# Performance work log

Hardware: AMD Instinct MI355X
Metric: run time of the kernel (lower is better)

The kernel has to match this reference:

```python
import jax, jax.numpy as jnp
import numpy as np
from jax import lax

G, CPG, KS, N = 8, 8, 3, 9  # groups, channels per group, kernel size, ks*ks


def conv2d(x, w, b=None, pad=1):
    y = lax.conv_general_dilated(x, w, (1, 1), [(pad, pad), (pad, pad)],
                                 dimension_numbers=('NCHW', 'OIHW', 'NCHW'))
    if b is not None:
        y = y + b[None, :, None, None]
    return y


def deform_group(x, f, pw, pb, mw, mb, cw):
    # x: sampled feature (anchor slice), f: offset source (motion slice); both (b,c,h,w)
    b, c, h, w = x.shape
    offset = conv2d(f, pw, pb)                      # (b, 2N, h, w)
    m = jax.nn.sigmoid(conv2d(f, mw, mb))           # (b, N, h, w) modulation
    off = jnp.transpose(offset, (0, 2, 3, 1))       # (b, h, w, 2N): first N rows(x), last N cols(y)
    rng = jnp.arange(-1, 2, dtype=x.dtype)
    pn_x = jnp.repeat(rng, KS)                      # kernel row offset, n = kr*3 + kc
    pn_y = jnp.tile(rng, KS)                        # kernel col offset
    p0_x = jnp.arange(1, h + 1, dtype=x.dtype)[:, None, None]  # base grid starts at 1 (padding=0 here)
    p0_y = jnp.arange(1, w + 1, dtype=x.dtype)[None, :, None]
    px = p0_x + pn_x + off[..., :N]                 # (b, h, w, N)
    py = p0_y + pn_y + off[..., N:]
    fx = jnp.floor(lax.stop_gradient(px))           # p.detach().floor() in the original
    fy = jnp.floor(lax.stop_gradient(py))
    qx_lt = jnp.clip(fx, 0, h - 1)
    qx_rb = jnp.clip(fx + 1, 0, h - 1)
    qy_lt = jnp.clip(fy, 0, w - 1)
    qy_rb = jnp.clip(fy + 1, 0, w - 1)
    px = jnp.clip(px, 0, h - 1)
    py = jnp.clip(py, 0, w - 1)
    g_lt = (1 + (qx_lt - px)) * (1 + (qy_lt - py))
    g_rb = (1 - (qx_rb - px)) * (1 - (qy_rb - py))
    g_lb = (1 + (qx_lt - px)) * (1 - (qy_rb - py))
    g_rt = (1 - (qx_rb - px)) * (1 + (qy_lt - py))
    x_flat = x.reshape(b, c, h * w)

    def gather(ix, iy):
        idx = (ix * w + iy).astype(jnp.int32).reshape(b, 1, -1)  # (b,1,h*w*N)
        return jnp.take_along_axis(x_flat, idx, axis=2).reshape(b, c, h, w, N)

    x_off = (g_lt[:, None] * gather(qx_lt, qy_lt) + g_rb[:, None] * gather(qx_rb, qy_rb)
             + g_lb[:, None] * gather(qx_lt, qy_rb) + g_rt[:, None] * gather(qx_rb, qy_lt))
    x_off = x_off * jnp.transpose(m, (0, 2, 3, 1))[:, None]      # apply modulation mask
    # fused equivalent of reshape to (b,c,h*3,w*3) + conv(k=3, stride=3, no bias)
    return jnp.einsum('bchwn,ocn->bohw', x_off, cw.reshape(cw.shape[0], c, N))


def reference(o, anchor, pw, pb, mw, mb, cw, w1, b1, w2, b2):
    b, C, h, w = anchor.shape
    xg = anchor.reshape(b, G, CPG, h, w).transpose(1, 0, 2, 3, 4)  # (G,b,c,h,w)
    fg = o.reshape(b, G, CPG, h, w).transpose(1, 0, 2, 3, 4)
    tg = jax.vmap(deform_group)(xg, fg, pw, pb, mw, mb, cw)        # (G,b,c,h,w)
    target = tg.transpose(1, 0, 2, 3, 4).reshape(b, C, h, w)
    target_ = jnp.concatenate([target, anchor], axis=1)            # (b,128,h,w)
    return target + conv2d(conv2d(target_, w1, b1), w2, b2)


def setup_inputs() -> dict:
    key = jax.random.key(0)
    ks = jax.random.split(key, 11)
    B, C, H, W = 4, 64, 128, 128
    return {
        'o': jax.random.normal(ks[0], (B, C, H, W), jnp.float32),
        'anchor': jax.random.normal(ks[1], (B, C, H, W), jnp.float32),
        'pw': jax.random.normal(ks[2], (G, 2 * N, CPG, 3, 3), jnp.float32) * 0.05,
        'pb': jax.random.normal(ks[3], (G, 2 * N), jnp.float32) * 0.05,
        'mw': jax.random.normal(ks[4], (G, N, CPG, 3, 3), jnp.float32) * 0.05,
        'mb': jax.random.normal(ks[5], (G, N), jnp.float32) * 0.05,
        'cw': jax.random.normal(ks[6], (G, CPG, CPG, 3, 3), jnp.float32) * 0.05,
        'w1': jax.random.normal(ks[7], (64, 128, 3, 3), jnp.float32) * 0.05,
        'b1': jax.random.normal(ks[8], (64,), jnp.float32) * 0.05,
        'w2': jax.random.normal(ks[9], (64, 64, 3, 3), jnp.float32) * 0.05,
        'b2': jax.random.normal(ks[10], (64,), jnp.float32) * 0.05,
    }
```

## Files before the change

### kernel.cpp

```cpp
#include <hip/hip_runtime.h>


typedef __attribute__((ext_vector_type(8))) short short8;
typedef __attribute__((ext_vector_type(4))) float float4v;
typedef __attribute__((ext_vector_type(2))) float float2v;

#define MFMA_B16(a, b, c) __builtin_amdgcn_mfma_f32_16x16x32_bf16(a, b, c, 0, 0, 0)

__device__ __forceinline__ ushort f2bf(float f) {
    union { float f; unsigned u; } v; v.f = f;
    unsigned r = v.u + 0x7FFFu + ((v.u >> 16) & 1u);
    return (ushort)(r >> 16);
}
__device__ __forceinline__ float bf2f(ushort h) {
    union { unsigned u; float f; } v; v.u = ((unsigned)h) << 16;
    return v.f;
}

__device__ __forceinline__ void tap_wo(int gy, int gx, int n,
                                       float ox, float oy, float mzv,
                                       float* W, int* O)
{
    int ky = n / 3, kx = n - ky * 3;
    float pxf = (float)(gy + ky) + ox;
    float pyf = (float)(gx + kx) + oy;
    float fx = floorf(pxf), fy = floorf(pyf);
    float qxl = fminf(fmaxf(fx, 0.f), 127.f);
    float qxr = fminf(fmaxf(fx + 1.f, 0.f), 127.f);
    float qyl = fminf(fmaxf(fy, 0.f), 127.f);
    float qyr = fminf(fmaxf(fy + 1.f, 0.f), 127.f);
    float pxc = fminf(fmaxf(pxf, 0.f), 127.f);
    float pyc = fminf(fmaxf(pyf, 0.f), 127.f);
    float glx = 1.f + (qxl - pxc), grx = 1.f - (qxr - pxc);
    float gly = 1.f + (qyl - pyc), gry = 1.f - (qyr - pyc);
    float mm = 1.f / (1.f + __expf(-mzv));
    W[0] = glx * gly * mm; W[1] = grx * gry * mm;
    W[2] = glx * gry * mm; W[3] = grx * gly * mm;
    int ixl = (int)qxl, ixr = (int)qxr, iyl = (int)qyl, iyr = (int)qyr;
    O[0] = ixl * 128 + iyl; O[1] = ixr * 128 + iyr;
    O[2] = ixl * 128 + iyr; O[3] = ixr * 128 + iyl;
}

__device__ __forceinline__ short8 interp4(const float* W, const short8* cv)
{
    union U { short8 s; uint4 u; };
    uint4 c[4];
    #pragma unroll
    for (int j = 0; j < 4; ++j) { U t; t.s = cv[j]; c[j] = t.u; }
    U out;
    #pragma unroll
    for (int p = 0; p < 4; ++p) {
        float2v acc = {0.f, 0.f};
        #pragma unroll
        for (int j = 0; j < 4; ++j) {
            unsigned d = (&c[j].x)[p];
            float2v cc = {__uint_as_float(d << 16),
                          __uint_as_float(d & 0xffff0000u)};
            float2v Wv = {W[j], W[j]};
            acc = __builtin_elementwise_fma(cc, Wv, acc);
        }
        unsigned u0 = __float_as_uint(acc.x), u1 = __float_as_uint(acc.y);
        (&out.u.x)[p] = __builtin_amdgcn_perm(u1, u0, 0x07060302u);
    }
    return out.s;
}

__global__ __launch_bounds__(256) void prep(
    const float* __restrict__ anchor,
    const float* __restrict__ w1, const float* __restrict__ w2,
    const float* __restrict__ pw, const float* __restrict__ pb,
    const float* __restrict__ mw, const float* __restrict__ mb,
    const float* __restrict__ cw,
    ushort* __restrict__ anc_g,
    ushort* __restrict__ rw1, ushort* __restrict__ rw2,
    ushort* __restrict__ rpwh, ushort* __restrict__ rpwl,
    ushort* __restrict__ rcw)
{
    const int blk = blockIdx.x;
    if (blk < 256) {
        int pix = (blk & 63) * 256 + threadIdx.x;
        int b = blk >> 6;
        ushort tmp[64];
        #pragma unroll
        for (int ch = 0; ch < 64; ++ch)
            tmp[ch] = f2bf(anchor[(((size_t)(b * 64 + ch)) << 14) + pix]);
        #pragma unroll
        for (int grp = 0; grp < 8; ++grp) {
            short8 v;
            #pragma unroll
            for (int j = 0; j < 8; ++j) v[j] = (short)tmp[grp * 8 + j];
            *(short8*)(anc_g + ((size_t)(b * 8 + grp)) * 131072 + (size_t)pix * 8) = v;
        }
        return;
    }
    int i = (blk - 256) * 256 + threadIdx.x;
    if (i < 73728) {
        int ic = i & 127, r = i >> 7, oc = r & 63, s = r >> 6;
        rw1[i] = f2bf(w1[(oc * 128 + ic) * 9 + s]);
    }
    if (i < 36864) {
        int ic = i & 63, r = i >> 6, oc = r & 63, s = r >> 6;
        rw2[i] = f2bf(w2[(oc * 64 + ic) * 9 + s]);
    }
    if (i < 24576) {
        int k = i % 96, r = i / 96, n = r & 31, g = r >> 5;
        float v = 0.f;
        if (k < 72) {
            int s = k >> 3, ic = k & 7;
            if (n < 18)      v = pw[((g * 18 + n) * 8 + ic) * 9 + s];
            else if (n < 27) v = mw[((g * 9 + (n - 18)) * 8 + ic) * 9 + s];
        } else if (k == 72) {
            if (n < 18)      v = pb[g * 18 + n];
            else if (n < 27) v = mb[g * 9 + (n - 18)];
        }
        ushort h = f2bf(v);
        rpwh[i] = h;
        rpwl[i] = f2bf(v - bf2f(h));
    }
    if (i < 12288) {
        int k = i % 96, r = i / 96, oc = r & 15, g = r >> 4;
        float v = 0.f;
        if (k < 72 && oc < 8) {
            int n = k >> 3, ic = k & 7;
            v = cw[((g * 8 + oc) * 8 + ic) * 9 + n];
        }
        rcw[i] = f2bf(v);
    }
}

__global__ __launch_bounds__(256, 4) void deform_mfma(
    const float* __restrict__ o, const ushort* __restrict__ anc_g,
    const ushort* __restrict__ rpwh, const ushort* __restrict__ rpwl,
    const ushort* __restrict__ rcw,
    ushort* __restrict__ xcat_g, float* __restrict__ target)
{
    const int tile = blockIdx.x, g = blockIdx.y, b = blockIdx.z;
    const int ty0 = (tile >> 3) * 16, tx0 = (tile & 7) * 16;
    const int tid = threadIdx.x, lane = tid & 63, wave = tid >> 6;
    const int l15 = lane & 15, quad = lane >> 4;

    __shared__ __align__(16) ushort sU[19008];
    ushort* slabh = sU;
    ushort* slabl = sU + 2592;
    float*  sOff  = (float*)((char*)sU + 10368);
    float*  sEp   = (float*)sU;

    for (int idx = tid; idx < 8 * 324; idx += 256) {
        int ic = idx / 324; int pix = idx - ic * 324;
        int r = pix / 18, c = pix - r * 18;
        int gy = ty0 + r - 1, gx = tx0 + c - 1;
        float v = 0.f;
        if ((unsigned)gy < 128u && (unsigned)gx < 128u)
            v = o[(((size_t)(b * 64 + g * 8 + ic)) << 14) + (gy << 7) + gx];
        ushort h = f2bf(v);
        slabh[pix * 8 + ic] = h;
        slabl[pix * 8 + ic] = f2bf(v - bf2f(h));
    }
    __syncthreads();

    float4v offacc[4][2] = {};
    #pragma unroll
    for (int ks = 0; ks < 3; ++ks) {
        short8 Bh[2], Bl[2];
        #pragma unroll
        for (int nf = 0; nf < 2; ++nf) {
            int off = (g * 32 + nf * 16 + l15) * 96 + ks * 32 + quad * 8;
            Bh[nf] = *(const short8*)(rpwh + off);
            Bl[nf] = *(const short8*)(rpwl + off);
        }
        short8 Ah[4], Al[4];
        if (ks < 2) {
            int s = ks * 4 + quad, sy = s / 3, sx = s - sy * 3;
            #pragma unroll
            for (int py = 0; py < 4; ++py) {
                int row = wave * 4 + py;
                int sl = ((row + sy) * 18 + l15 + sx) * 8;
                Ah[py] = *(const short8*)(&slabh[sl]);
                Al[py] = *(const short8*)(&slabl[sl]);
            }
        } else {
            #pragma unroll
            for (int py = 0; py < 4; ++py) {
                short8 zh = {0, 0, 0, 0, 0, 0, 0, 0};
                short8 zl = {0, 0, 0, 0, 0, 0, 0, 0};
                if (quad == 0) {
                    int row = wave * 4 + py;
                    int sl = ((row + 2) * 18 + l15 + 2) * 8;
                    zh = *(const short8*)(&slabh[sl]);
                    zl = *(const short8*)(&slabl[sl]);
                } else if (quad == 1) {
                    zh[0] = (short)0x3F80;
                }
                Ah[py] = zh; Al[py] = zl;
            }
        }
        #pragma unroll
        for (int py = 0; py < 4; ++py)
            #pragma unroll
            for (int nf = 0; nf < 2; ++nf) {
                offacc[py][nf] = MFMA_B16(Ah[py], Bh[nf], offacc[py][nf]);
                offacc[py][nf] = MFMA_B16(Ah[py], Bl[nf], offacc[py][nf]);
                offacc[py][nf] = MFMA_B16(Al[py], Bh[nf], offacc[py][nf]);
            }
    }
    #pragma unroll
    for (int py = 0; py < 4; ++py) {
        int p0 = (wave * 4 + py) * 16 + quad * 4;
        #pragma unroll
        for (int nf = 0; nf < 2; ++nf) {
            int ch = nf * 16 + l15;
            if (ch < 27) {
                #pragma unroll
                for (int reg = 0; reg < 4; ++reg)
                    sOff[(p0 + reg) * 27 + ch] = offacc[py][nf][reg];
            }
        }
    }

    short8 Bw[3];
    #pragma unroll
    for (int ks = 0; ks < 3; ++ks)
        Bw[ks] = *(const short8*)(rcw + ((g * 16 + l15) * 96 + ks * 32 + quad * 8));

    const ushort* gb = anc_g + ((size_t)(b * 8 + g)) * 131072;
    const int n1 = quad, n2 = quad + 4;
    float4v cacc[4] = {};
    #pragma unroll
    for (int py = 0; py < 4; ++py) {
        int prow = wave * 4 + py;
        int p = prow * 16 + l15;
        int gy = ty0 + prow, gx = tx0 + l15;

        float W[8]; int O[8];
        tap_wo(gy, gx, n1, sOff[p * 27 + n1], sOff[p * 27 + 9 + n1],
               sOff[p * 27 + 18 + n1], &W[0], &O[0]);
        tap_wo(gy, gx, n2, sOff[p * 27 + n2], sOff[p * 27 + 9 + n2],
               sOff[p * 27 + 18 + n2], &W[4], &O[4]);
        short8 cv[8];
        #pragma unroll
        for (int j = 0; j < 8; ++j)
            cv[j] = *(const short8*)(gb + (size_t)O[j] * 8);
        short8 A0 = interp4(&W[0], &cv[0]);
        short8 A1 = interp4(&W[4], &cv[4]);
        short8 A2 = {0, 0, 0, 0, 0, 0, 0, 0};
        if (quad == 0) {
            float W2[4]; int O2[4];
            tap_wo(gy, gx, 8, sOff[p * 27 + 8], sOff[p * 27 + 17],
                   sOff[p * 27 + 26], W2, O2);
            short8 c2[4];
            #pragma unroll
            for (int j = 0; j < 4; ++j)
                c2[j] = *(const short8*)(gb + (size_t)O2[j] * 8);
            A2 = interp4(W2, c2);
        }
        cacc[py] = MFMA_B16(A0, Bw[0], cacc[py]);
        cacc[py] = MFMA_B16(A1, Bw[1], cacc[py]);
        cacc[py] = MFMA_B16(A2, Bw[2], cacc[py]);
    }

    __syncthreads();
    #pragma unroll
    for (int py = 0; py < 4; ++py) {
        if (l15 < 8) {
            #pragma unroll
            for (int reg = 0; reg < 4; ++reg)
                sEp[((wave * 4 + py) * 16 + quad * 4 + reg) * 8 + l15] = cacc[py][reg];
        }
    }
    __syncthreads();
    {
        const int p = tid;
        const int gy = ty0 + (p >> 4), gx = tx0 + (p & 15);
        float res[8];
        #pragma unroll
        for (int oc = 0; oc < 8; ++oc) res[oc] = sEp[p * 8 + oc];
        short8 pk;
        #pragma unroll
        for (int oc = 0; oc < 8; ++oc) pk[oc] = (short)f2bf(res[oc]);
        *(short8*)(xcat_g + ((size_t)(b * 8 + g)) * 131072
                   + (size_t)((gy << 7) + gx) * 8) = pk;
        #pragma unroll
        for (int oc = 0; oc < 8; ++oc)
            target[(((size_t)(b * 64 + g * 8 + oc)) << 14) + (gy << 7) + gx] = res[oc];
    }
}

__global__ __launch_bounds__(256, 4) void conv1_mfma(
    const ushort* __restrict__ xg, const ushort* __restrict__ ag,
    const ushort* __restrict__ rw1, const float* __restrict__ b1,
    ushort* __restrict__ t1)
{
    const int patch = blockIdx.x, b = blockIdx.y;
    const int px0 = (patch & 7) * 16, py0 = (patch >> 3) * 4;
    const int tid = threadIdx.x, lane = tid & 63, wave = tid >> 6;
    const int ohalf = wave & 1, rhalf = wave >> 1;
    const int l15 = lane & 15, quad = lane >> 4;

    __shared__ __align__(16) ushort sA[108 * 128];

    for (int task = tid; task < 1728; task += 256) {
        int grp = task / 108, pix = task - grp * 108;
        int r = pix / 18, c = pix - r * 18;
        int gy = py0 + r - 1, gx = px0 + c - 1;
        short8 v = {0, 0, 0, 0, 0, 0, 0, 0};
        if ((unsigned)gy < 128u && (unsigned)gx < 128u) {
            const ushort* plane = ((grp < 8) ? xg : ag)
                                  + ((size_t)(b * 8 + (grp & 7))) * 131072;
            v = *(const short8*)(plane + (size_t)((gy << 7) + gx) * 8);
        }
        *(short8*)(&sA[pix * 128 + ((grp ^ (pix & 15)) * 8)]) = v;
    }
    __syncthreads();

    float4v acc[2][2] = {};
    #pragma unroll
    for (int ks = 0; ks < 4; ++ks) {
        #pragma unroll
        for (int ky = 0; ky < 3; ++ky) {
            short8 Bf[3][2];
            #pragma unroll
            for (int kx = 0; kx < 3; ++kx)
                #pragma unroll
                for (int nf = 0; nf < 2; ++nf) {
                    int oc = ohalf * 32 + nf * 16 + l15;
                    Bf[kx][nf] = *(const short8*)(rw1 +
                        (((ky * 3 + kx) * 64 + oc) * 128 + ks * 32 + quad * 8));
                }
            #pragma unroll
            for (int t = 0; t < 2; ++t) {
                int row = rhalf * 2 + t + ky;
                #pragma unroll
                for (int kx = 0; kx < 3; ++kx) {
                    int pix = row * 18 + l15 + kx;
                    short8 A = *(const short8*)(&sA[pix * 128 +
                        (((ks * 4 + quad) ^ (pix & 15)) * 8)]);
                    #pragma unroll
                    for (int nf = 0; nf < 2; ++nf)
                        acc[t][nf] = MFMA_B16(A, Bf[kx][nf], acc[t][nf]);
                }
            }
        }
    }
    const size_t nbase = ((size_t)b) << 20;
    #pragma unroll
    for (int nf = 0; nf < 2; ++nf) {
        int oc = ohalf * 32 + nf * 16 + l15;
        float bias = b1[oc];
        #pragma unroll
        for (int t = 0; t < 2; ++t) {
            int gy = py0 + rhalf * 2 + t;
            #pragma unroll
            for (int reg = 0; reg < 4; ++reg) {
                int gx = px0 + quad * 4 + reg;
                t1[nbase + (size_t)((gy << 7) + gx) * 64 + oc] = f2bf(acc[t][nf][reg] + bias);
            }
        }
    }
}

__global__ __launch_bounds__(256, 4) void conv2_mfma(
    const ushort* __restrict__ t1, const ushort* __restrict__ rw2,
    const float* __restrict__ b2, float* outres)
{
    const int patch = blockIdx.x, b = blockIdx.y;
    const int px0 = (patch & 7) * 16, py0 = (patch >> 3) * 4;
    const int tid = threadIdx.x, lane = tid & 63, wave = tid >> 6;
    const int ohalf = wave & 1, rhalf = wave >> 1;
    const int l15 = lane & 15, quad = lane >> 4;

    __shared__ __align__(16) ushort sX[108 * 64];

    const size_t nbase = ((size_t)b) << 20;
    for (int task = tid; task < 864; task += 256) {
        int grp = task / 108, pix = task - grp * 108;
        int r = pix / 18, c = pix - r * 18;
        int gy = py0 + r - 1, gx = px0 + c - 1;
        short8 v = {0, 0, 0, 0, 0, 0, 0, 0};
        if ((unsigned)gy < 128u && (unsigned)gx < 128u)
            v = *(const short8*)(t1 + nbase + (size_t)((gy << 7) + gx) * 64 + grp * 8);
        *(short8*)(&sX[pix * 64 + ((grp ^ (pix & 7)) * 8)]) = v;
    }
    __syncthreads();

    float4v acc[2][2] = {};
    #pragma unroll
    for (int ks = 0; ks < 2; ++ks) {
        #pragma unroll
        for (int ky = 0; ky < 3; ++ky) {
            short8 Aw[3][2];
            #pragma unroll
            for (int kx = 0; kx < 3; ++kx)
                #pragma unroll
                for (int mf = 0; mf < 2; ++mf) {
                    int oc = ohalf * 32 + mf * 16 + l15;
                    Aw[kx][mf] = *(const short8*)(rw2 +
                        (((ky * 3 + kx) * 64 + oc) * 64 + ks * 32 + quad * 8));
                }
            #pragma unroll
            for (int t = 0; t < 2; ++t) {
                int row = rhalf * 2 + t + ky;
                #pragma unroll
                for (int kx = 0; kx < 3; ++kx) {
                    int pix = row * 18 + l15 + kx;
                    short8 Bx = *(const short8*)(&sX[pix * 64 +
                        (((ks * 4 + quad) ^ (pix & 7)) * 8)]);
                    #pragma unroll
                    for (int mf = 0; mf < 2; ++mf)
                        acc[mf][t] = MFMA_B16(Aw[kx][mf], Bx, acc[mf][t]);
                }
            }
        }
    }
    #pragma unroll
    for (int mf = 0; mf < 2; ++mf)
        #pragma unroll
        for (int reg = 0; reg < 4; ++reg) {
            int oc = ohalf * 32 + mf * 16 + quad * 4 + reg;
            float bias = b2[oc];
            #pragma unroll
            for (int t = 0; t < 2; ++t) {
                int gy = py0 + rhalf * 2 + t, gx = px0 + l15;
                size_t idx = (((size_t)(b * 64 + oc)) << 14) + (gy << 7) + gx;
                outres[idx] = acc[mf][t][reg] + bias + outres[idx];
            }
        }
}

extern "C" void kernel_launch(void* const* d_in, const int* in_sizes, int n_in,
                              void* d_out, int out_size, void* d_ws, size_t ws_size,
                              hipStream_t stream) {
    const float* o      = (const float*)d_in[0];
    const float* anchor = (const float*)d_in[1];
    const float* pw     = (const float*)d_in[2];
    const float* pb     = (const float*)d_in[3];
    const float* mw     = (const float*)d_in[4];
    const float* mb     = (const float*)d_in[5];
    const float* cw     = (const float*)d_in[6];
    const float* w1     = (const float*)d_in[7];
    const float* b1     = (const float*)d_in[8];
    const float* w2     = (const float*)d_in[9];
    const float* b2     = (const float*)d_in[10];
    float* out = (float*)d_out;

    char* ws = (char*)d_ws;
    ushort* anc_g  = (ushort*)(ws);
    ushort* xcat_g = (ushort*)(ws + 8388608);
    ushort* t1b    = (ushort*)(ws + 16777216);
    char*   wsm    = ws + 25165824;
    ushort* rw1p   = (ushort*)(wsm);
    ushort* rw2p   = (ushort*)(wsm + 147456);
    ushort* rpwh   = (ushort*)(wsm + 147456 + 73728);
    ushort* rpwl   = (ushort*)(wsm + 147456 + 73728 + 49152);
    ushort* rcwp   = (ushort*)(wsm + 147456 + 73728 + 98304);

    prep<<<544, 256, 0, stream>>>(anchor, w1, w2, pw, pb, mw, mb, cw,
                                  anc_g, rw1p, rw2p, rpwh, rpwl, rcwp);
    deform_mfma<<<dim3(64, 8, 4), 256, 0, stream>>>(o, anc_g, rpwh, rpwl, rcwp,
                                                    xcat_g, out );
    conv1_mfma<<<dim3(256, 4), 256, 0, stream>>>(xcat_g, anc_g, rw1p, b1, t1b);
    conv2_mfma<<<dim3(256, 4), 256, 0, stream>>>(t1b, rw2p, b2, out);
}
```

Measured before the change: 201.6 us.

## Enlarge conv tiles to 8 rows, repack weights per k-slice, stage conv1 output

The two convolution kernels now cover 16x8-pixel patches instead of 16x4, so each block reuses every loaded weight fragment over twice as many MFMAs, and the grid shrinks to 128 blocks per batch. conv1 loads its 128 input channels in two 64-channel phases into a padded (stride 72) LDS slab in place of the XOR-swizzled one. Its bf16 results are staged through LDS so t1 is written with 16-byte vector stores instead of scattered 2-byte stores. All packed weight buffers are reordered so each 32-wide k-slice is contiguous, making the fragment loads more compact. The trade-offs are more accumulator registers, an extra barrier pass, and fewer blocks to fill the GPU.

```diff
diff --git a/kernel.cpp b/kernel.cpp
--- a/kernel.cpp
+++ b/kernel.cpp
@@ -95,15 +95,18 @@
     }
     int i = (blk - 256) * 256 + threadIdx.x;
     if (i < 73728) {
-        int ic = i & 127, r = i >> 7, oc = r & 63, s = r >> 6;
+        int kk = i & 31, r = i >> 5, oc = r & 63, r2 = r >> 6;
+        int ks = r2 & 3, s = r2 >> 2, ic = ks * 32 + kk;
         rw1[i] = f2bf(w1[(oc * 128 + ic) * 9 + s]);
     }
     if (i < 36864) {
-        int ic = i & 63, r = i >> 6, oc = r & 63, s = r >> 6;
+        int kk = i & 31, r = i >> 5, oc = r & 63, r2 = r >> 6;
+        int ks = r2 & 1, s = r2 >> 1, ic = ks * 32 + kk;
         rw2[i] = f2bf(w2[(oc * 64 + ic) * 9 + s]);
     }
     if (i < 24576) {
-        int k = i % 96, r = i / 96, n = r & 31, g = r >> 5;
+        int kk = i & 31, r = i >> 5, n = r & 31, r2 = r >> 5;
+        int ks = r2 % 3, g = r2 / 3, k = ks * 32 + kk;
         float v = 0.f;
         if (k < 72) {
             int s = k >> 3, ic = k & 7;
@@ -118,7 +121,8 @@
         rpwl[i] = f2bf(v - bf2f(h));
     }
     if (i < 12288) {
-        int k = i % 96, r = i / 96, oc = r & 15, g = r >> 4;
+        int kk = i & 31, r = i >> 5, oc = r & 15, r2 = r >> 4;
+        int ks = r2 % 3, g = r2 / 3, k = ks * 32 + kk;
         float v = 0.f;
         if (k < 72 && oc < 8) {
             int n = k >> 3, ic = k & 7;
@@ -164,7 +168,7 @@
         short8 Bh[2], Bl[2];
         #pragma unroll
         for (int nf = 0; nf < 2; ++nf) {
-            int off = (g * 32 + nf * 16 + l15) * 96 + ks * 32 + quad * 8;
+            int off = ((g * 3 + ks) * 32 + nf * 16 + l15) * 32 + quad * 8;
             Bh[nf] = *(const short8*)(rpwh + off);
             Bl[nf] = *(const short8*)(rpwl + off);
         }
@@ -220,7 +224,7 @@
     short8 Bw[3];
     #pragma unroll
     for (int ks = 0; ks < 3; ++ks)
-        Bw[ks] = *(const short8*)(rcw + ((g * 16 + l15) * 96 + ks * 32 + quad * 8));
+        Bw[ks] = *(const short8*)(rcw + (((g * 3 + ks) * 16 + l15) * 32 + quad * 8));
 
     const ushort* gb = anc_g + ((size_t)(b * 8 + g)) * 131072;
     const int n1 = quad, n2 = quad + 4;
@@ -291,98 +295,112 @@
     ushort* __restrict__ t1)
 {
     const int patch = blockIdx.x, b = blockIdx.y;
-    const int px0 = (patch & 7) * 16, py0 = (patch >> 3) * 4;
+    const int px0 = (patch & 7) * 16, py0 = (patch >> 3) * 8;
+    const int tid = threadIdx.x, lane = tid & 63, wave = tid >> 6;
+    const int mhalf = wave & 1, nhalf = wave >> 1;
+    const int l15 = lane & 15, quad = lane >> 4;
+
+    __shared__ __align__(16) ushort sA[180 * 72];
+
+    float4v acc[4][2] = {};
+    #pragma unroll
+    for (int ph = 0; ph < 2; ++ph) {
+        if (ph) __syncthreads();
+        const ushort* src = (ph == 0) ? xg : ag;
+        for (int task = tid; task < 1440; task += 256) {
+            int grp = task / 180, pix = task - grp * 180;
+            int r = pix / 18, c = pix - r * 18;
+            int gy = py0 + r - 1, gx = px0 + c - 1;
+            short8 v = {0, 0, 0, 0, 0, 0, 0, 0};
+            if ((unsigned)gy < 128u && (unsigned)gx < 128u) {
+                const ushort* plane = src + ((size_t)(b * 8 + grp)) * 131072;
+                v = *(const short8*)(plane + (size_t)((gy << 7) + gx) * 8);
+            }
+            *(short8*)(&sA[pix * 72 + grp * 8]) = v;
+        }
+        __syncthreads();
+
+        #pragma unroll
+        for (int ks2 = 0; ks2 < 2; ++ks2) {
+            const int ks = ph * 2 + ks2;
+            #pragma unroll
+            for (int ky = 0; ky < 3; ++ky) {
+                short8 Bf[3][2];
+                #pragma unroll
+                for (int kx = 0; kx < 3; ++kx)
+                    #pragma unroll
+                    for (int nf = 0; nf < 2; ++nf) {
+                        int oc = nhalf * 32 + nf * 16 + l15;
+                        Bf[kx][nf] = *(const short8*)(rw1 +
+                            ((((ky * 3 + kx) * 4 + ks) * 64 + oc) * 32 + quad * 8));
+                    }
+                #pragma unroll
+                for (int py = 0; py < 4; ++py) {
+                    int slabrow = mhalf * 4 + py + ky;
+                    #pragma unroll
+                    for (int kx = 0; kx < 3; ++kx) {
+                        short8 A = *(const short8*)(&sA[(slabrow * 18 + l15 + kx) * 72
+                                                        + ks2 * 32 + quad * 8]);
+                        #pragma unroll
+                        for (int nf = 0; nf < 2; ++nf)
+                            acc[py][nf] = MFMA_B16(A, Bf[kx][nf], acc[py][nf]);
+                    }
+                }
+            }
+        }
+    }
+    __syncthreads();
+    ushort* sE = sA;
+    #pragma unroll
+    for (int nf = 0; nf < 2; ++nf) {
+        int oc = nhalf * 32 + nf * 16 + l15;
+        float bias = b1[oc];
+        #pragma unroll
+        for (int py = 0; py < 4; ++py) {
+            int row = mhalf * 4 + py;
+            #pragma unroll
+            for (int reg = 0; reg < 4; ++reg)
+                sE[(row * 16 + quad * 4 + reg) * 64 + oc] = f2bf(acc[py][nf][reg] + bias);
+        }
+    }
+    __syncthreads();
+    {
+        const size_t nbase = ((size_t)b) << 20;
+        int pix = tid >> 1, half = tid & 1;
+        int gy = py0 + (pix >> 4), gx = px0 + (pix & 15);
+        ushort* dst = t1 + nbase + (size_t)((gy << 7) + gx) * 64 + half * 32;
+        const ushort* sp = sE + pix * 64 + half * 32;
+        #pragma unroll
+        for (int j = 0; j < 4; ++j)
+            *(short8*)(dst + j * 8) = *(const short8*)(sp + j * 8);
+    }
+}
+
+__global__ __launch_bounds__(256, 4) void conv2_mfma(
+    const ushort* __restrict__ t1, const ushort* __restrict__ rw2,
+    const float* __restrict__ b2, float* outres)
+{
+    const int patch = blockIdx.x, b = blockIdx.y;
+    const int px0 = (patch & 7) * 16, py0 = (patch >> 3) * 8;
     const int tid = threadIdx.x, lane = tid & 63, wave = tid >> 6;
     const int ohalf = wave & 1, rhalf = wave >> 1;
     const int l15 = lane & 15, quad = lane >> 4;
 
-    __shared__ __align__(16) ushort sA[108 * 128];
-
-    for (int task = tid; task < 1728; task += 256) {
-        int grp = task / 108, pix = task - grp * 108;
-        int r = pix / 18, c = pix - r * 18;
-        int gy = py0 + r - 1, gx = px0 + c - 1;
-        short8 v = {0, 0, 0, 0, 0, 0, 0, 0};
-        if ((unsigned)gy < 128u && (unsigned)gx < 128u) {
-            const ushort* plane = ((grp < 8) ? xg : ag)
-                                  + ((size_t)(b * 8 + (grp & 7))) * 131072;
-            v = *(const short8*)(plane + (size_t)((gy << 7) + gx) * 8);
-        }
-        *(short8*)(&sA[pix * 128 + ((grp ^ (pix & 15)) * 8)]) = v;
-    }
-    __syncthreads();
-
-    float4v acc[2][2] = {};
-    #pragma unroll
-    for (int ks = 0; ks < 4; ++ks) {
-        #pragma unroll
-        for (int ky = 0; ky < 3; ++ky) {
-            short8 Bf[3][2];
-            #pragma unroll
-            for (int kx = 0; kx < 3; ++kx)
-                #pragma unroll
-                for (int nf = 0; nf < 2; ++nf) {
-                    int oc = ohalf * 32 + nf * 16 + l15;
-                    Bf[kx][nf] = *(const short8*)(rw1 +
-                        (((ky * 3 + kx) * 64 + oc) * 128 + ks * 32 + quad * 8));
-                }
-            #pragma unroll
-            for (int t = 0; t < 2; ++t) {
-                int row = rhalf * 2 + t + ky;
-                #pragma unroll
-                for (int kx = 0; kx < 3; ++kx) {
-                    int pix = row * 18 + l15 + kx;
-                    short8 A = *(const short8*)(&sA[pix * 128 +
-                        (((ks * 4 + quad) ^ (pix & 15)) * 8)]);
-                    #pragma unroll
-                    for (int nf = 0; nf < 2; ++nf)
-                        acc[t][nf] = MFMA_B16(A, Bf[kx][nf], acc[t][nf]);
-                }
-            }
-        }
-    }
+    __shared__ __align__(16) ushort sX[180 * 72];
+
     const size_t nbase = ((size_t)b) << 20;
-    #pragma unroll
-    for (int nf = 0; nf < 2; ++nf) {
-        int oc = ohalf * 32 + nf * 16 + l15;
-        float bias = b1[oc];
-        #pragma unroll
-        for (int t = 0; t < 2; ++t) {
-            int gy = py0 + rhalf * 2 + t;
-            #pragma unroll
-            for (int reg = 0; reg < 4; ++reg) {
-                int gx = px0 + quad * 4 + reg;
-                t1[nbase + (size_t)((gy << 7) + gx) * 64 + oc] = f2bf(acc[t][nf][reg] + bias);
-            }
-        }
-    }
-}
-
-__global__ __launch_bounds__(256, 4) void conv2_mfma(
-    const ushort* __restrict__ t1, const ushort* __restrict__ rw2,
-    const float* __restrict__ b2, float* outres)
-{
-    const int patch = blockIdx.x, b = blockIdx.y;
-    const int px0 = (patch & 7) * 16, py0 = (patch >> 3) * 4;
-    const int tid = threadIdx.x, lane = tid & 63, wave = tid >> 6;
-    const int ohalf = wave & 1, rhalf = wave >> 1;
-    const int l15 = lane & 15, quad = lane >> 4;
-
-    __shared__ __align__(16) ushort sX[108 * 64];
-
-    const size_t nbase = ((size_t)b) << 20;
-    for (int task = tid; task < 864; task += 256) {
-        int grp = task / 108, pix = task - grp * 108;
+    for (int task = tid; task < 1440; task += 256) {
+        int pix = task >> 3, grp = task & 7;
         int r = pix / 18, c = pix - r * 18;
         int gy = py0 + r - 1, gx = px0 + c - 1;
         short8 v = {0, 0, 0, 0, 0, 0, 0, 0};
         if ((unsigned)gy < 128u && (unsigned)gx < 128u)
             v = *(const short8*)(t1 + nbase + (size_t)((gy << 7) + gx) * 64 + grp * 8);
-        *(short8*)(&sX[pix * 64 + ((grp ^ (pix & 7)) * 8)]) = v;
-    }
-    __syncthreads();
-
-    float4v acc[2][2] = {};
+        *(short8*)(&sX[pix * 72 + grp * 8]) = v;
+    }
+    __syncthreads();
+
+    float4v acc[2][4] = {};
     #pragma unroll
     for (int ks = 0; ks < 2; ++ks) {
         #pragma unroll
@@ -394,19 +412,18 @@
                 for (int mf = 0; mf < 2; ++mf) {
                     int oc = ohalf * 32 + mf * 16 + l15;
                     Aw[kx][mf] = *(const short8*)(rw2 +
-                        (((ky * 3 + kx) * 64 + oc) * 64 + ks * 32 + quad * 8));
+                        ((((ky * 3 + kx) * 2 + ks) * 64 + oc) * 32 + quad * 8));
                 }
             #pragma unroll
-            for (int t = 0; t < 2; ++t) {
-                int row = rhalf * 2 + t + ky;
+            for (int py = 0; py < 4; ++py) {
+                int slabrow = rhalf * 4 + py + ky;
                 #pragma unroll
                 for (int kx = 0; kx < 3; ++kx) {
-                    int pix = row * 18 + l15 + kx;
-                    short8 Bx = *(const short8*)(&sX[pix * 64 +
-                        (((ks * 4 + quad) ^ (pix & 7)) * 8)]);
+                    short8 Bx = *(const short8*)(&sX[(slabrow * 18 + l15 + kx) * 72
+                                                     + ks * 32 + quad * 8]);
                     #pragma unroll
                     for (int mf = 0; mf < 2; ++mf)
-                        acc[mf][t] = MFMA_B16(Aw[kx][mf], Bx, acc[mf][t]);
+                        acc[mf][py] = MFMA_B16(Aw[kx][mf], Bx, acc[mf][py]);
                 }
             }
         }
@@ -418,10 +435,10 @@
             int oc = ohalf * 32 + mf * 16 + quad * 4 + reg;
             float bias = b2[oc];
             #pragma unroll
-            for (int t = 0; t < 2; ++t) {
-                int gy = py0 + rhalf * 2 + t, gx = px0 + l15;
+            for (int py = 0; py < 4; ++py) {
+                int gy = py0 + rhalf * 4 + py, gx = px0 + l15;
                 size_t idx = (((size_t)(b * 64 + oc)) << 14) + (gy << 7) + gx;
-                outres[idx] = acc[mf][t][reg] + bias + outres[idx];
+                outres[idx] = acc[mf][py][reg] + bias + outres[idx];
             }
         }
 }
@@ -457,6 +474,6 @@
                                   anc_g, rw1p, rw2p, rpwh, rpwl, rcwp);
     deform_mfma<<<dim3(64, 8, 4), 256, 0, stream>>>(o, anc_g, rpwh, rpwl, rcwp,
                                                     xcat_g, out );
-    conv1_mfma<<<dim3(256, 4), 256, 0, stream>>>(xcat_g, anc_g, rw1p, b1, t1b);
-    conv2_mfma<<<dim3(256, 4), 256, 0, stream>>>(t1b, rw2p, b2, out);
-}
+    conv1_mfma<<<dim3(128, 4), 256, 0, stream>>>(xcat_g, anc_g, rw1p, b1, t1b);
+    conv2_mfma<<<dim3(128, 4), 256, 0, stream>>>(t1b, rw2p, b2, out);
+}
```

Result: faster. 175.1 us (-13.1%).
